# Performance work log

Measured on AMD Instinct MI355X. Metric: run time of the kernel, lower is better.

## Reference

```python
import jax, jax.numpy as jnp
import numpy as np

NUM_ITEMS = 50000
NUM_USERS = 16384   # static number of user segments (total_user universe)
H0 = 512            # encoder_hidden_size[0]
LAT = 256           # bottleneck (encoder_hidden_size[-1] / decoder_hidden_size[0])
N = 262144          # observed interactions
NT = 262144         # target interactions


def setup_inputs() -> dict:
    key = jax.random.key(0)
    ks = jax.random.split(key, 14)

    def glorot(k, shape):
        fan_in, fan_out = shape[1], shape[0]
        lim = np.sqrt(6.0 / (fan_in + fan_out)).astype(np.float32)
        return jax.random.uniform(k, shape, jnp.float32, -lim, lim)

    return {
        "user": jax.random.randint(ks[0], (N,), 0, NUM_USERS, jnp.int32),
        "item": jax.random.randint(ks[1], (N,), 0, NUM_ITEMS, jnp.int32),
        "rating": jax.random.normal(ks[2], (N,), jnp.float32),
        "target_user": jax.random.randint(ks[3], (NT,), 0, NUM_USERS, jnp.int32),
        "target_item": jax.random.randint(ks[4], (NT,), 0, NUM_ITEMS, jnp.int32),
        "target_rating": jax.random.normal(ks[5], (NT,), jnp.float32),
        # encoder_linear: Linear(num_items, H0)
        "W_enc": glorot(ks[6], (H0, NUM_ITEMS)),
        "b_enc": jnp.zeros((H0,), jnp.float32),
        # Encoder: Linear(H0, LAT) + Tanh
        "W1": glorot(ks[7], (LAT, H0)),
        "b1": jnp.zeros((LAT,), jnp.float32),
        # Decoder: Linear(LAT, H0) + Tanh
        "W2": glorot(ks[8], (H0, LAT)),
        "b2": jnp.zeros((H0,), jnp.float32),
        # decoder_linear: Linear(H0, num_items)
        "W_dec": glorot(ks[9], (NUM_ITEMS, H0)),
        "b_dec": jnp.zeros((NUM_ITEMS,), jnp.float32),
    }


def reference(user, item, rating, target_user, target_item, target_rating,
              W_enc, b_enc, W1, b1, W2, b2, W_dec, b_dec):
    # --- encoder: gather item weight rows, scale by rating, segment-sum per user ---
    # rows: [N, H0] gather from W_enc.T ([NUM_ITEMS, H0])
    rows = W_enc.T[item] * rating[:, None]
    # per-user aggregation over the full user universe (equivalent to the
    # torch unique/sort/index_add path: users with no interactions get 0 -> tanh(bias))
    agg = jax.ops.segment_sum(rows, user, num_segments=NUM_USERS)  # [U, H0]
    x = jnp.tanh(agg + b_enc)
    # --- small dense tanh MLP encoder/decoder ---
    encoded = jnp.tanh(x @ W1.T + b1)          # [U, LAT]
    decoded = jnp.tanh(encoded @ W2.T + b2)    # [U, H0] (dropout = identity, eval mode)
    # --- decoder: gather user codes & item decoder rows, rowwise dot ---
    g = decoded[target_user]                   # [NT, H0]
    w = W_dec[target_item]                     # [NT, H0]
    pred = jnp.sum(g * w, axis=-1) + b_dec[target_item]  # [NT]
    loss = jnp.mean((pred - target_rating) ** 2)
    return pred, loss
```

## Files before the change

### kernel.cpp

```cpp
#include <hip/hip_runtime.h>
#include <hip/hip_bf16.h>
#include <math.h>

#define NUM_ITEMS 50000
#define NUM_USERS 16384
#define H0 512
#define LAT 256

typedef __attribute__((ext_vector_type(8))) short short8;
typedef __attribute__((ext_vector_type(4))) float floatx4;

__device__ __forceinline__ unsigned short f2bf(float f) {
    union { float f; unsigned i; } u; u.f = f;
    unsigned r = u.i + 0x7fff + ((u.i >> 16) & 1);
    return (unsigned short)(r >> 16);
}
__device__ __forceinline__ float bfhi(unsigned v) {
    union { unsigned i; float f; } u; u.i = v & 0xffff0000u; return u.f;
}
__device__ __forceinline__ float bflo(unsigned v) {
    union { unsigned i; float f; } u; u.i = v << 16; return u.f;
}

__global__ void transpose_kernel(const float* __restrict__ src, unsigned short* __restrict__ dst) {
    __shared__ float tile[32][33];
    int tx = threadIdx.x, ty = threadIdx.y;
    int x0 = blockIdx.x * 32, y0 = blockIdx.y * 32;
    int x = x0 + tx;
    if (x < NUM_ITEMS) {
#pragma unroll
        for (int j = 0; j < 32; j += 8)
            tile[ty + j][tx] = src[(size_t)(y0 + ty + j) * NUM_ITEMS + x];
    }
    __syncthreads();
#pragma unroll
    for (int j = 0; j < 32; j += 8) {
        int it = x0 + ty + j;
        if (it < NUM_ITEMS)
            dst[(size_t)it * H0 + y0 + tx] = f2bf(tile[tx][ty + j]);
    }
}

__global__ void f2bf_kernel(const float* __restrict__ src, unsigned short* __restrict__ dst, int n) {
    int i = blockIdx.x * blockDim.x + threadIdx.x;
    if (i < n) dst[i] = f2bf(src[i]);
}

__global__ void count_kernel(const int* __restrict__ user, int* __restrict__ cnt, int n) {
    int i = blockIdx.x * blockDim.x + threadIdx.x;
    if (i < n) atomicAdd(&cnt[user[i]], 1);
}

__global__ void scan_kernel(const int* __restrict__ cnt, int* __restrict__ offs,
                            int* __restrict__ cursor) {
    __shared__ int ssum[1024];
    int t = threadIdx.x;
    int base = t * 16;
    int local[16];
    int s = 0;
#pragma unroll
    for (int j = 0; j < 16; ++j) { local[j] = s; s += cnt[base + j]; }
    ssum[t] = s;
    __syncthreads();
    for (int off = 1; off < 1024; off <<= 1) {
        int v = (t >= off) ? ssum[t - off] : 0;
        __syncthreads();
        ssum[t] += v;
        __syncthreads();
    }
    int excl = (t == 0) ? 0 : ssum[t - 1];
#pragma unroll
    for (int j = 0; j < 16; ++j) {
        int o = excl + local[j];
        offs[base + j] = o;
        cursor[base + j] = o;
    }
}

__global__ void scatter_kernel(const int* __restrict__ user, const int* __restrict__ item,
                               const float* __restrict__ rating, int* __restrict__ cursor,
                               int* __restrict__ s_item, float* __restrict__ s_rat, int n) {
    int i = blockIdx.x * blockDim.x + threadIdx.x;
    if (i < n) {
        int u = user[i];
        int pos = atomicAdd(&cursor[u], 1);
        s_item[pos] = item[i];
        s_rat[pos] = rating[i];
    }
}

__global__ __launch_bounds__(256) void agg_kernel(const unsigned short* __restrict__ wtb,
                                                  const int* __restrict__ offs,
                                                  const int* __restrict__ ends,
                                                  const int* __restrict__ s_item,
                                                  const float* __restrict__ s_rat,
                                                  const float* __restrict__ b_enc,
                                                  unsigned short* __restrict__ xb) {
    __shared__ float red[3 * 512];
    int u = blockIdx.x;
    int tid = threadIdx.x;
    int g = tid >> 6, lane = tid & 63;
    float acc[8] = {};
    int j0 = offs[u], j1 = ends[u];
    for (int j = j0 + g; j < j1; j += 4) {
        int it = s_item[j];
        float r = s_rat[j];
        uint4 v = ((const uint4*)(wtb + (size_t)it * H0))[lane];
        acc[0] += bflo(v.x) * r; acc[1] += bfhi(v.x) * r;
        acc[2] += bflo(v.y) * r; acc[3] += bfhi(v.y) * r;
        acc[4] += bflo(v.z) * r; acc[5] += bfhi(v.z) * r;
        acc[6] += bflo(v.w) * r; acc[7] += bfhi(v.w) * r;
    }
    if (g) {
        float4* rp = (float4*)red + (size_t)(g - 1) * 128 + lane * 2;
        rp[0] = make_float4(acc[0], acc[1], acc[2], acc[3]);
        rp[1] = make_float4(acc[4], acc[5], acc[6], acc[7]);
    }
    __syncthreads();
    if (g == 0) {
#pragma unroll
        for (int h = 0; h < 3; ++h) {
            const float* rp = red + h * 512 + lane * 8;
#pragma unroll
            for (int e = 0; e < 8; ++e) acc[e] += rp[e];
        }
        float4 b0 = ((const float4*)b_enc)[lane * 2];
        float4 b1 = ((const float4*)b_enc)[lane * 2 + 1];
        unsigned short o[8];
        o[0] = f2bf(tanhf(acc[0] + b0.x)); o[1] = f2bf(tanhf(acc[1] + b0.y));
        o[2] = f2bf(tanhf(acc[2] + b0.z)); o[3] = f2bf(tanhf(acc[3] + b0.w));
        o[4] = f2bf(tanhf(acc[4] + b1.x)); o[5] = f2bf(tanhf(acc[5] + b1.y));
        o[6] = f2bf(tanhf(acc[6] + b1.z)); o[7] = f2bf(tanhf(acc[7] + b1.w));
        uint4 pk;
        pk.x = (unsigned)o[0] | ((unsigned)o[1] << 16);
        pk.y = (unsigned)o[2] | ((unsigned)o[3] << 16);
        pk.z = (unsigned)o[4] | ((unsigned)o[5] << 16);
        pk.w = (unsigned)o[6] | ((unsigned)o[7] << 16);
        ((uint4*)(xb + (size_t)u * H0))[lane] = pk;
    }
}

__global__ __launch_bounds__(256) void gemm_mfma(const unsigned short* __restrict__ A,
                                                 const unsigned short* __restrict__ B,
                                                 const float* __restrict__ bias,
                                                 unsigned short* __restrict__ C,
                                                 int Nn, int K) {
    __shared__ unsigned short Ash[128 * 32];
    __shared__ unsigned short Bsh[128 * 32];
    int tid = threadIdx.x;
    int wid = tid >> 6, lane = tid & 63;
    int wave_m = wid & 1, wave_n = wid >> 1;
    int quad = lane >> 4, l16 = lane & 15;
    int m0 = blockIdx.x * 128, n0 = blockIdx.y * 128;
    floatx4 acc[4][4] = {};

    int srow = lane >> 2;
    int scol = (lane & 3) * 8;
    for (int k0 = 0; k0 < K; k0 += 32) {
#pragma unroll
        for (int i = 0; i < 2; ++i) {
            int c = wid * 2 + i;
            int row = c * 16 + srow;
            const unsigned short* ga = A + (size_t)(m0 + row) * K + k0 + scol;
            const unsigned short* gb = B + (size_t)(n0 + row) * K + k0 + scol;
            __builtin_amdgcn_global_load_lds(
                (const __attribute__((address_space(1))) void*)ga,
                (__attribute__((address_space(3))) void*)((__attribute__((address_space(3))) char*)Ash + c * 1024),
                16, 0, 0);
            __builtin_amdgcn_global_load_lds(
                (const __attribute__((address_space(1))) void*)gb,
                (__attribute__((address_space(3))) void*)((__attribute__((address_space(3))) char*)Bsh + c * 1024),
                16, 0, 0);
        }
        __syncthreads();
        short8 af[4], bfr[4];
#pragma unroll
        for (int i = 0; i < 4; ++i) {
            int ml = wave_m * 64 + i * 16 + l16;
            af[i] = ((const short8*)Ash)[ml * 4 + quad];
            int nl = wave_n * 64 + i * 16 + l16;
            bfr[i] = ((const short8*)Bsh)[nl * 4 + quad];
        }
#pragma unroll
        for (int i = 0; i < 4; ++i)
#pragma unroll
            for (int j = 0; j < 4; ++j)
                acc[i][j] = __builtin_amdgcn_mfma_f32_16x16x32_bf16(af[i], bfr[j], acc[i][j], 0, 0, 0);
        __syncthreads();
    }
#pragma unroll
    for (int j = 0; j < 4; ++j) {
        int col = n0 + wave_n * 64 + j * 16 + l16;
        float bv = bias[col];
#pragma unroll
        for (int i = 0; i < 4; ++i) {
            int rowb = m0 + wave_m * 64 + i * 16 + quad * 4;
#pragma unroll
            for (int r = 0; r < 4; ++r)
                C[(size_t)(rowb + r) * Nn + col] = f2bf(tanhf(acc[i][j][r] + bv));
        }
    }
}

__global__ __launch_bounds__(256) void predict_kernel(const unsigned short* __restrict__ dec_b,
                                                      const float* __restrict__ W_dec,
                                                      const float* __restrict__ b_dec,
                                                      const int* __restrict__ t_user,
                                                      const int* __restrict__ t_item,
                                                      const float* __restrict__ t_rating,
                                                      float* __restrict__ pred,
                                                      float* __restrict__ partials, int NT) {
    __shared__ float wsum[4];
    int wid = threadIdx.x >> 6, lane = threadIdx.x & 63;
    int base = (blockIdx.x * 4 + wid) * 4;
    float sq = 0.f;
    int tu[4], ti[4];
    uint4 gv[4];
    float4 wv0[4], wv1[4];
#pragma unroll
    for (int t = 0; t < 4; ++t) {
        int idx = min(base + t, NT - 1);
        tu[t] = t_user[idx];
        ti[t] = t_item[idx];
    }
#pragma unroll
    for (int t = 0; t < 4; ++t) {
        gv[t] = ((const uint4*)(dec_b + (size_t)tu[t] * H0))[lane];
        const float4* w = (const float4*)(W_dec + (size_t)ti[t] * H0);
        wv0[t] = w[lane * 2];
        wv1[t] = w[lane * 2 + 1];
    }
#pragma unroll
    for (int t = 0; t < 4; ++t) {
        float s = bflo(gv[t].x) * wv0[t].x + bfhi(gv[t].x) * wv0[t].y
                + bflo(gv[t].y) * wv0[t].z + bfhi(gv[t].y) * wv0[t].w
                + bflo(gv[t].z) * wv1[t].x + bfhi(gv[t].z) * wv1[t].y
                + bflo(gv[t].w) * wv1[t].z + bfhi(gv[t].w) * wv1[t].w;
#pragma unroll
        for (int off = 32; off; off >>= 1) s += __shfl_xor(s, off, 64);
        if (lane == 0 && base + t < NT) {
            float p = s + b_dec[ti[t]];
            pred[base + t] = p;
            float d = p - t_rating[base + t];
            sq += d * d;
        }
    }
    if (lane == 0) wsum[wid] = sq;
    __syncthreads();
    if (threadIdx.x == 0) partials[blockIdx.x] = wsum[0] + wsum[1] + wsum[2] + wsum[3];
}

__global__ void loss_reduce(const float* __restrict__ partials, float* __restrict__ out_loss,
                            int nPart, float invNT) {
    __shared__ float s[256];
    int t = threadIdx.x;
    float a = 0.f;
    for (int i = t; i < nPart; i += 256) a += partials[i];
    s[t] = a;
    __syncthreads();
    for (int off = 128; off; off >>= 1) {
        if (t < off) s[t] += s[t + off];
        __syncthreads();
    }
    if (t == 0) out_loss[0] = s[0] * invNT;
}

extern "C" void kernel_launch(void* const* d_in, const int* in_sizes, int n_in,
                              void* d_out, int out_size, void* d_ws, size_t ws_size,
                              hipStream_t stream) {
    const int* user = (const int*)d_in[0];
    const int* item = (const int*)d_in[1];
    const float* rating = (const float*)d_in[2];
    const int* t_user = (const int*)d_in[3];
    const int* t_item = (const int*)d_in[4];
    const float* t_rating = (const float*)d_in[5];
    const float* W_enc = (const float*)d_in[6];
    const float* b_enc = (const float*)d_in[7];
    const float* W1 = (const float*)d_in[8];
    const float* b1 = (const float*)d_in[9];
    const float* W2 = (const float*)d_in[10];
    const float* b2 = (const float*)d_in[11];
    const float* W_dec = (const float*)d_in[12];
    const float* b_dec = (const float*)d_in[13];
    const int N = in_sizes[0];
    const int NT = in_sizes[3];

    char* ws = (char*)d_ws;
    size_t off = 0;
    auto alloc = [&](size_t bytes) {
        void* p = ws + off;
        off = (off + bytes + 255) & ~(size_t)255;
        return p;
    };
    unsigned short* wtb = (unsigned short*)alloc((size_t)NUM_ITEMS * H0 * 2);
    unsigned short* xb = (unsigned short*)alloc((size_t)NUM_USERS * H0 * 2);
    unsigned short* enc_b = (unsigned short*)alloc((size_t)NUM_USERS * LAT * 2);
    unsigned short* dec_b = (unsigned short*)alloc((size_t)NUM_USERS * H0 * 2);
    unsigned short* w1b = (unsigned short*)alloc((size_t)LAT * H0 * 2);
    unsigned short* w2b = (unsigned short*)alloc((size_t)H0 * LAT * 2);
    int* cnt = (int*)alloc((size_t)NUM_USERS * 4);
    int* offs = (int*)alloc((size_t)NUM_USERS * 4);
    int* cursor = (int*)alloc((size_t)NUM_USERS * 4);
    int* s_item = (int*)alloc((size_t)N * 4);
    float* s_rat = (float*)alloc((size_t)N * 4);
    const int predBlocks = (NT + 15) / 16;
    float* partials = (float*)alloc((size_t)predBlocks * 4);

    float* pred = (float*)d_out;
    float* loss = pred + NT;

    hipMemsetAsync(cnt, 0, (size_t)NUM_USERS * 4, stream);
    transpose_kernel<<<dim3((NUM_ITEMS + 31) / 32, H0 / 32), dim3(32, 8), 0, stream>>>(W_enc, wtb);
    count_kernel<<<(N + 255) / 256, 256, 0, stream>>>(user, cnt, N);
    scan_kernel<<<1, 1024, 0, stream>>>(cnt, offs, cursor);
    scatter_kernel<<<(N + 255) / 256, 256, 0, stream>>>(user, item, rating, cursor, s_item, s_rat, N);
    f2bf_kernel<<<(LAT * H0 + 255) / 256, 256, 0, stream>>>(W1, w1b, LAT * H0);
    f2bf_kernel<<<(H0 * LAT + 255) / 256, 256, 0, stream>>>(W2, w2b, H0 * LAT);
    agg_kernel<<<NUM_USERS, 256, 0, stream>>>(wtb, offs, cursor, s_item, s_rat, b_enc, xb);
    gemm_mfma<<<dim3(NUM_USERS / 128, LAT / 128), 256, 0, stream>>>(xb, w1b, b1, enc_b, LAT, H0);
    gemm_mfma<<<dim3(NUM_USERS / 128, H0 / 128), 256, 0, stream>>>(enc_b, w2b, b2, dec_b, H0, LAT);
    predict_kernel<<<predBlocks, 256, 0, stream>>>(dec_b, W_dec, b_dec, t_user, t_item, t_rating,
                                                   pred, partials, NT);
    loss_reduce<<<1, 256, 0, stream>>>(partials, loss, predBlocks, 1.0f / NT);
}
```

Before: 475.9 us.

## Sort target interactions by item so predict reads W_dec rows with locality

Adds a counting sort of the target interactions by item, done alongside the existing user sort, so the predict kernel walks targets grouped by item and reuses W_dec rows through cache. Predictions are scattered back to their original positions through a stored index. It also merges the two weight-conversion launches into one kernel. The cost is extra atomics, a second scan block and extra scatter traffic for the four sorted target arrays.

```diff
diff --git a/kernel.cpp b/kernel.cpp
--- a/kernel.cpp
+++ b/kernel.cpp
@@ -4,6 +4,7 @@
 
 #define NUM_ITEMS 50000
 #define NUM_USERS 16384
+#define ITEM_BINS 50176
 #define H0 512
 #define LAT 256
 
@@ -41,25 +42,28 @@
     }
 }
 
-__global__ void f2bf_kernel(const float* __restrict__ src, unsigned short* __restrict__ dst, int n) {
+__global__ void f2bf2_kernel(const float* __restrict__ a, unsigned short* __restrict__ da,
+                             const float* __restrict__ b, unsigned short* __restrict__ db, int n) {
     int i = blockIdx.x * blockDim.x + threadIdx.x;
-    if (i < n) dst[i] = f2bf(src[i]);
-}
-
-__global__ void count_kernel(const int* __restrict__ user, int* __restrict__ cnt, int n) {
+    if (i < n) da[i] = f2bf(a[i]);
+    else { int j = i - n; if (j < n) db[j] = f2bf(b[j]); }
+}
+
+__global__ void count_kernel(const int* __restrict__ user, int* __restrict__ cntU,
+                             const int* __restrict__ t_item, int* __restrict__ cntI,
+                             int n, int nt) {
     int i = blockIdx.x * blockDim.x + threadIdx.x;
-    if (i < n) atomicAdd(&cnt[user[i]], 1);
-}
-
-__global__ void scan_kernel(const int* __restrict__ cnt, int* __restrict__ offs,
-                            int* __restrict__ cursor) {
+    if (i < n) atomicAdd(&cntU[user[i]], 1);
+    if (i < nt) atomicAdd(&cntI[t_item[i]], 1);
+}
+
+__device__ void scan_block(const int* __restrict__ cnt, int* __restrict__ offs,
+                           int* __restrict__ cursor, int per) {
     __shared__ int ssum[1024];
     int t = threadIdx.x;
-    int base = t * 16;
-    int local[16];
+    int base = t * per;
     int s = 0;
-#pragma unroll
-    for (int j = 0; j < 16; ++j) { local[j] = s; s += cnt[base + j]; }
+    for (int j = 0; j < per; ++j) s += cnt[base + j];
     ssum[t] = s;
     __syncthreads();
     for (int off = 1; off < 1024; off <<= 1) {
@@ -68,24 +72,42 @@
         ssum[t] += v;
         __syncthreads();
     }
-    int excl = (t == 0) ? 0 : ssum[t - 1];
-#pragma unroll
-    for (int j = 0; j < 16; ++j) {
-        int o = excl + local[j];
-        offs[base + j] = o;
-        cursor[base + j] = o;
-    }
+    int run = (t == 0) ? 0 : ssum[t - 1];
+    for (int j = 0; j < per; ++j) {
+        offs[base + j] = run;
+        cursor[base + j] = run;
+        run += cnt[base + j];
+    }
+}
+
+__global__ void scan_kernel(const int* __restrict__ cntU, int* __restrict__ offsU, int* __restrict__ curU,
+                            const int* __restrict__ cntI, int* __restrict__ offsI, int* __restrict__ curI) {
+    if (blockIdx.x == 0) scan_block(cntU, offsU, curU, NUM_USERS / 1024);
+    else scan_block(cntI, offsI, curI, ITEM_BINS / 1024);
 }
 
 __global__ void scatter_kernel(const int* __restrict__ user, const int* __restrict__ item,
-                               const float* __restrict__ rating, int* __restrict__ cursor,
-                               int* __restrict__ s_item, float* __restrict__ s_rat, int n) {
+                               const float* __restrict__ rating, int* __restrict__ curU,
+                               int* __restrict__ s_item, float* __restrict__ s_rat,
+                               const int* __restrict__ t_user, const int* __restrict__ t_item,
+                               const float* __restrict__ t_rating, int* __restrict__ curI,
+                               int* __restrict__ st_user, int* __restrict__ st_item,
+                               float* __restrict__ st_rat, int* __restrict__ st_idx,
+                               int n, int nt) {
     int i = blockIdx.x * blockDim.x + threadIdx.x;
     if (i < n) {
         int u = user[i];
-        int pos = atomicAdd(&cursor[u], 1);
+        int pos = atomicAdd(&curU[u], 1);
         s_item[pos] = item[i];
         s_rat[pos] = rating[i];
+    }
+    if (i < nt) {
+        int it = t_item[i];
+        int pos = atomicAdd(&curI[it], 1);
+        st_user[pos] = t_user[i];
+        st_item[pos] = it;
+        st_rat[pos] = t_rating[i];
+        st_idx[pos] = i;
     }
 }
 
@@ -205,9 +227,10 @@
 __global__ __launch_bounds__(256) void predict_kernel(const unsigned short* __restrict__ dec_b,
                                                       const float* __restrict__ W_dec,
                                                       const float* __restrict__ b_dec,
-                                                      const int* __restrict__ t_user,
-                                                      const int* __restrict__ t_item,
-                                                      const float* __restrict__ t_rating,
+                                                      const int* __restrict__ st_user,
+                                                      const int* __restrict__ st_item,
+                                                      const float* __restrict__ st_rat,
+                                                      const int* __restrict__ st_idx,
                                                       float* __restrict__ pred,
                                                       float* __restrict__ partials, int NT) {
     __shared__ float wsum[4];
@@ -220,8 +243,8 @@
 #pragma unroll
     for (int t = 0; t < 4; ++t) {
         int idx = min(base + t, NT - 1);
-        tu[t] = t_user[idx];
-        ti[t] = t_item[idx];
+        tu[t] = st_user[idx];
+        ti[t] = st_item[idx];
     }
 #pragma unroll
     for (int t = 0; t < 4; ++t) {
@@ -239,9 +262,10 @@
 #pragma unroll
         for (int off = 32; off; off >>= 1) s += __shfl_xor(s, off, 64);
         if (lane == 0 && base + t < NT) {
+            int idx = base + t;
             float p = s + b_dec[ti[t]];
-            pred[base + t] = p;
-            float d = p - t_rating[base + t];
+            pred[st_idx[idx]] = p;
+            float d = p - st_rat[idx];
             sq += d * d;
         }
     }
@@ -298,28 +322,37 @@
     unsigned short* dec_b = (unsigned short*)alloc((size_t)NUM_USERS * H0 * 2);
     unsigned short* w1b = (unsigned short*)alloc((size_t)LAT * H0 * 2);
     unsigned short* w2b = (unsigned short*)alloc((size_t)H0 * LAT * 2);
-    int* cnt = (int*)alloc((size_t)NUM_USERS * 4);
-    int* offs = (int*)alloc((size_t)NUM_USERS * 4);
-    int* cursor = (int*)alloc((size_t)NUM_USERS * 4);
+    int* cntU = (int*)alloc((size_t)(NUM_USERS + ITEM_BINS) * 4);
+    int* cntI = cntU + NUM_USERS;
+    int* offsU = (int*)alloc((size_t)NUM_USERS * 4);
+    int* curU = (int*)alloc((size_t)NUM_USERS * 4);
+    int* offsI = (int*)alloc((size_t)ITEM_BINS * 4);
+    int* curI = (int*)alloc((size_t)ITEM_BINS * 4);
     int* s_item = (int*)alloc((size_t)N * 4);
     float* s_rat = (float*)alloc((size_t)N * 4);
+    int* st_user = (int*)alloc((size_t)NT * 4);
+    int* st_item = (int*)alloc((size_t)NT * 4);
+    float* st_rat = (float*)alloc((size_t)NT * 4);
+    int* st_idx = (int*)alloc((size_t)NT * 4);
     const int predBlocks = (NT + 15) / 16;
     float* partials = (float*)alloc((size_t)predBlocks * 4);
 
     float* pred = (float*)d_out;
     float* loss = pred + NT;
 
-    hipMemsetAsync(cnt, 0, (size_t)NUM_USERS * 4, stream);
+    const int maxNNT = N > NT ? N : NT;
+    hipMemsetAsync(cntU, 0, (size_t)(NUM_USERS + ITEM_BINS) * 4, stream);
+    count_kernel<<<(maxNNT + 255) / 256, 256, 0, stream>>>(user, cntU, t_item, cntI, N, NT);
+    scan_kernel<<<2, 1024, 0, stream>>>(cntU, offsU, curU, cntI, offsI, curI);
+    scatter_kernel<<<(maxNNT + 255) / 256, 256, 0, stream>>>(
+        user, item, rating, curU, s_item, s_rat,
+        t_user, t_item, t_rating, curI, st_user, st_item, st_rat, st_idx, N, NT);
     transpose_kernel<<<dim3((NUM_ITEMS + 31) / 32, H0 / 32), dim3(32, 8), 0, stream>>>(W_enc, wtb);
-    count_kernel<<<(N + 255) / 256, 256, 0, stream>>>(user, cnt, N);
-    scan_kernel<<<1, 1024, 0, stream>>>(cnt, offs, cursor);
-    scatter_kernel<<<(N + 255) / 256, 256, 0, stream>>>(user, item, rating, cursor, s_item, s_rat, N);
-    f2bf_kernel<<<(LAT * H0 + 255) / 256, 256, 0, stream>>>(W1, w1b, LAT * H0);
-    f2bf_kernel<<<(H0 * LAT + 255) / 256, 256, 0, stream>>>(W2, w2b, H0 * LAT);
-    agg_kernel<<<NUM_USERS, 256, 0, stream>>>(wtb, offs, cursor, s_item, s_rat, b_enc, xb);
+    f2bf2_kernel<<<(2 * LAT * H0 + 255) / 256, 256, 0, stream>>>(W1, w1b, W2, w2b, LAT * H0);
+    agg_kernel<<<NUM_USERS, 256, 0, stream>>>(wtb, offsU, curU, s_item, s_rat, b_enc, xb);
     gemm_mfma<<<dim3(NUM_USERS / 128, LAT / 128), 256, 0, stream>>>(xb, w1b, b1, enc_b, LAT, H0);
     gemm_mfma<<<dim3(NUM_USERS / 128, H0 / 128), 256, 0, stream>>>(enc_b, w2b, b2, dec_b, H0, LAT);
-    predict_kernel<<<predBlocks, 256, 0, stream>>>(dec_b, W_dec, b_dec, t_user, t_item, t_rating,
-                                                   pred, partials, NT);
+    predict_kernel<<<predBlocks, 256, 0, stream>>>(dec_b, W_dec, b_dec, st_user, st_item, st_rat,
+                                                   st_idx, pred, partials, NT);
     loss_reduce<<<1, 256, 0, stream>>>(partials, loss, predBlocks, 1.0f / NT);
 }
```

Measured after the change: 472.8 us. No clear change (-0.6%).
